# Optimization experiments

Measured on AMD Instinct MI355X. Metric: run time of the kernel, lower is better.

## Reference

```python
import jax, jax.numpy as jnp
import numpy as np


def setup_inputs() -> dict:
    key = jax.random.key(0)
    k1, k2 = jax.random.split(key)
    K, D = 512, 64
    x = jax.random.normal(k1, (64, D, 32, 32), dtype=jnp.float32)
    # torch init: uniform(-1/k, 1/k)
    weight = jax.random.uniform(k2, (D, K), dtype=jnp.float32, minval=-1.0 / K, maxval=1.0 / K)
    return {"x": x, "weight": weight}


def reference(x, weight):
    # x: [B, d, *spatial]; weight: [d, k]
    B, d = x.shape[0], x.shape[1]
    spatial = x.shape[2:]
    xf = x.reshape(B, d, -1)                      # [B, d, N]
    x2 = jnp.sum(xf * xf, axis=1)                 # [B, N]
    w2 = jnp.sum(weight * weight, axis=0)         # [k]
    dots = jnp.einsum('bdn,dk->bnk', xf, weight)  # [B, N, k]
    dist = x2[..., None] - 2.0 * dots + w2        # [B, N, k]
    argmin = jnp.argmin(dist, axis=-1)            # [B, N]
    quantized = jnp.take(weight.T, argmin, axis=0)          # [B, N, d]
    quantized = jnp.moveaxis(quantized.reshape(B, *spatial, d), -1, 1)  # [B, d, *spatial]
    return quantized, argmin.reshape(B, *spatial)
```

## Files before the change

### kernel.cpp

```cpp
#include <hip/hip_runtime.h>

#define KCODES 512
#define DDIM   64
#define NPIX   1024
#define QELEMS (64 * DDIM * NPIX)
#define PXB    64
#define FLAG_GAP 4e-5f

typedef float f32x4 __attribute__((ext_vector_type(4)));
typedef short bf16x8 __attribute__((ext_vector_type(8)));
typedef unsigned int u32;
typedef u32 u32x4 __attribute__((ext_vector_type(4)));


__device__ __forceinline__ bf16x8 pack_hi(const float* f) {
  u32x4 wds;
#pragma unroll
  for (int p = 0; p < 4; ++p) {
    u32 u0 = __float_as_uint(f[2 * p]);
    u32 u1 = __float_as_uint(f[2 * p + 1]);
    wds[p] = (u0 >> 16) | (u1 & 0xffff0000u);
  }
  return __builtin_bit_cast(bf16x8, wds);
}
__device__ __forceinline__ bf16x8 pack_lo(const float* f) {
  u32x4 wds;
#pragma unroll
  for (int p = 0; p < 4; ++p) {
    float r0 = f[2 * p]     - __uint_as_float(__float_as_uint(f[2 * p])     & 0xffff0000u);
    float r1 = f[2 * p + 1] - __uint_as_float(__float_as_uint(f[2 * p + 1]) & 0xffff0000u);
    wds[p] = (__float_as_uint(r0) >> 16) | (__float_as_uint(r1) & 0xffff0000u);
  }
  return __builtin_bit_cast(bf16x8, wds);
}

__global__ void vq_prep(const float* __restrict__ w,
                        float* __restrict__ w2f_g,
                        bf16x8* __restrict__ frag) {
#pragma clang fp contract(off)
  const int blk = blockIdx.x;
  if (blk == 32) {
    int k = threadIdx.x;
    if (k < KCODES) {
      float s = 0.0f;
      for (int d = 0; d < DDIM; ++d) {
        float v = w[d * KCODES + k];
        float p = v * v;
        s = s + p;
      }
      w2f_g[k] = s;
    }
    return;
  }
  if (threadIdx.x >= 256) return;
  const int cg   = blk;
  const int t    = threadIdx.x >> 6;
  const int lane = threadIdx.x & 63;
  const int code = cg * 16 + (lane & 15);
  const int h    = t & 1;
  float f[8];
#pragma unroll
  for (int j = 0; j < 8; ++j)
    f[j] = w[(h * 32 + (lane >> 4) * 8 + j) * KCODES + code];
  frag[(cg * 4 + t) * 64 + lane] = (t < 2) ? pack_hi(f) : pack_lo(f);
}

__global__ __launch_bounds__(256) void vq_kernel(
    const float* __restrict__ x, const float* __restrict__ w,
    const float* __restrict__ w2f_g, const bf16x8* __restrict__ frag,
    float* __restrict__ qout, float* __restrict__ aout) {
#pragma clang fp contract(off)

  __shared__ float  xs[DDIM][PXB + 1];
  __shared__ float  w2fs[KCODES];
  __shared__ int    skm[PXB];

  const int tid  = threadIdx.x;
  const int lane = tid & 63;
  const int lr   = lane & 15;
  const int lg   = lane >> 4;
  const int wid  = __builtin_amdgcn_readfirstlane(tid >> 6);
  const int b    = blockIdx.x >> 4;
  const int n0   = (blockIdx.x & 15) * PXB;
  const size_t pixbase = (size_t)blockIdx.x * PXB;
  const int px0  = wid * 16;

  {
    const float* xp = x + (size_t)b * (DDIM * NPIX) + n0;
#pragma unroll
    for (int dd = 0; dd < 16; ++dd) {
      int d = dd * 4 + wid;
      xs[d][lane] = xp[(size_t)d * NPIX + lane];
    }
  }
  w2fs[tid]       = w2f_g[tid];
  w2fs[tid + 256] = w2f_g[tid + 256];
  __syncthreads();

  bf16x8 bxh[2], bxl[2];
#pragma unroll
  for (int h = 0; h < 2; ++h) {
    float f[8];
#pragma unroll
    for (int j = 0; j < 8; ++j)
      f[j] = xs[h * 32 + lg * 8 + j][px0 + lr];
    bxh[h] = pack_hi(f);
    bxl[h] = pack_lo(f);
  }

  float m1 = 3.4e38f, m2 = 3.4e38f;
  int   i1 = 0;
#pragma unroll 2
  for (int cg = 0; cg < 32; ++cg) {
    const bf16x8* fr = frag + (size_t)cg * 4 * 64 + lane;
    bf16x8 awh0 = fr[0];
    bf16x8 awh1 = fr[64];
    bf16x8 awl0 = fr[128];
    bf16x8 awl1 = fr[192];

    f32x4 acc = {0.f, 0.f, 0.f, 0.f};
    acc = __builtin_amdgcn_mfma_f32_16x16x32_bf16(awh0, bxh[0], acc, 0, 0, 0);
    acc = __builtin_amdgcn_mfma_f32_16x16x32_bf16(awh1, bxh[1], acc, 0, 0, 0);
    acc = __builtin_amdgcn_mfma_f32_16x16x32_bf16(awl0, bxh[0], acc, 0, 0, 0);
    acc = __builtin_amdgcn_mfma_f32_16x16x32_bf16(awl1, bxh[1], acc, 0, 0, 0);
    acc = __builtin_amdgcn_mfma_f32_16x16x32_bf16(awh0, bxl[0], acc, 0, 0, 0);
    acc = __builtin_amdgcn_mfma_f32_16x16x32_bf16(awh1, bxl[1], acc, 0, 0, 0);
    acc = __builtin_amdgcn_mfma_f32_16x16x32_bf16(awl0, bxl[0], acc, 0, 0, 0);
    acc = __builtin_amdgcn_mfma_f32_16x16x32_bf16(awl1, bxl[1], acc, 0, 0, 0);
#pragma unroll
    for (int r = 0; r < 4; ++r) {
      int code = cg * 16 + lg * 4 + r;
      float s = w2fs[code] - 2.0f * acc[r];
      bool lt = s < m1;
      float om1 = m1;
      m2 = lt ? om1 : fminf(s, m2);
      m1 = lt ? s : m1;
      i1 = lt ? code : i1;
    }
  }

#pragma unroll
  for (int mi = 0; mi < 2; ++mi) {
    int mask = mi ? 32 : 16;
    float pm1 = __shfl_xor(m1, mask);
    float pm2 = __shfl_xor(m2, mask);
    int   pi1 = __shfl_xor(i1, mask);
    if (pm1 < m1) { m2 = fminf(m1, pm2); m1 = pm1; i1 = pi1; }
    else          { m2 = fminf(m2, pm1); }
  }
  if (lg == 0) skm[px0 + lr] = i1;

  unsigned long long bal = __ballot(m2 - m1 < FLAG_GAP);
  unsigned int fmask = (unsigned int)(bal & 0xFFFFu);

  while (fmask) {
    const int Lr = __builtin_ctz(fmask);
    fmask &= fmask - 1;
    const int L = px0 + Lr;
    float x2L = 0.0f;
    for (int d = 0; d < DDIM; ++d) {
      float xv = xs[d][L];
      float p = xv * xv;
      x2L = x2L + p;
    }
    const int k0 = lane * 8;
    float dots[8];
#pragma unroll
    for (int c = 0; c < 8; ++c) dots[c] = 0.f;
    for (int d = 0; d < DDIM; d += 4) {
      f32x4 wa[4][2];
      float xv[4];
#pragma unroll
      for (int u = 0; u < 4; ++u) {
        const float* wr = w + (size_t)(d + u) * KCODES + k0;
        wa[u][0] = *reinterpret_cast<const f32x4*>(wr);
        wa[u][1] = *reinterpret_cast<const f32x4*>(wr + 4);
        xv[u] = xs[d + u][L];
      }
#pragma unroll
      for (int u = 0; u < 4; ++u) {
#pragma unroll
        for (int c = 0; c < 4; ++c) {
          float p = xv[u] * wa[u][0][c];
          dots[c] = dots[c] + p;
        }
#pragma unroll
        for (int c = 0; c < 4; ++c) {
          float p = xv[u] * wa[u][1][c];
          dots[c + 4] = dots[c + 4] + p;
        }
      }
    }
    float bv = 3.4e38f;
    int   bi = 0;
#pragma unroll
    for (int c = 0; c < 8; ++c) {
      float t  = x2L - 2.0f * dots[c];
      float s2 = t + w2fs[k0 + c];
      if (s2 < bv) { bv = s2; bi = k0 + c; }
    }
#pragma unroll
    for (int off = 1; off < 64; off <<= 1) {
      float ov = __shfl_xor(bv, off);
      int   oi = __shfl_xor(bi, off);
      if (ov < bv || (ov == bv && oi < bi)) { bv = ov; bi = oi; }
    }
    if (lane == 0) skm[L] = bi;
  }

  if (lg == 0) aout[pixbase + px0 + lr] = (float)skm[px0 + lr];

  __syncthreads();

  {
    float* qp = qout + (size_t)b * (DDIM * NPIX) + n0;
#pragma unroll
    for (int i = 0; i < 16; ++i) {
      int d  = (tid >> 6) + i * 4;
      int px = tid & 63;
      qp[(size_t)d * NPIX + px] = w[d * KCODES + skm[px]];
    }
  }
}

extern "C" void kernel_launch(void* const* d_in, const int* in_sizes, int n_in,
                              void* d_out, int out_size, void* d_ws, size_t ws_size,
                              hipStream_t stream) {
  const float* x = (const float*)d_in[0];
  const float* w = (const float*)d_in[1];
  float* qout = (float*)d_out;
  float* aout = (float*)d_out + QELEMS;

  char*   wsb   = (char*)d_ws;
  float*  w2f_g = (float*)wsb;
  bf16x8* frag  = (bf16x8*)(wsb + 4096);

  vq_prep<<<33, 512, 0, stream>>>(w, w2f_g, frag);
  vq_kernel<<<(65536 / PXB), 256, 0, stream>>>(x, w, w2f_g, frag, qout, aout);
}
```

Baseline: 47.51 us.

## Halve pixels per block and split codebook search across wave pairs

Each block now handles 32 pixels instead of 64. Every pair of waves shares a 16-pixel tile and each wave scans half of the codebook groups. The two partial top-2 results are merged through shared memory, and the exact fp32 fallback for near-tie pixels is split between the pair. This doubles the grid size and raises occupancy through launch_bounds(256,8), aiming at better latency hiding, at the cost of an extra barrier, a shared-memory merge, and narrower 32-wide global loads and stores.

```diff
diff --git a/kernel.cpp b/kernel.cpp
--- a/kernel.cpp
+++ b/kernel.cpp
@@ -4,7 +4,7 @@
 #define DDIM   64
 #define NPIX   1024
 #define QELEMS (64 * DDIM * NPIX)
-#define PXB    64
+#define PXB    32
 #define FLAG_GAP 4e-5f
 
 typedef float f32x4 __attribute__((ext_vector_type(4)));
@@ -65,7 +65,7 @@
   frag[(cg * 4 + t) * 64 + lane] = (t < 2) ? pack_hi(f) : pack_lo(f);
 }
 
-__global__ __launch_bounds__(256) void vq_kernel(
+__global__ __launch_bounds__(256, 8) void vq_kernel(
     const float* __restrict__ x, const float* __restrict__ w,
     const float* __restrict__ w2f_g, const bf16x8* __restrict__ frag,
     float* __restrict__ qout, float* __restrict__ aout) {
@@ -73,6 +73,8 @@
 
   __shared__ float  xs[DDIM][PXB + 1];
   __shared__ float  w2fs[KCODES];
+  __shared__ float  hm1[2][PXB], hm2[2][PXB];
+  __shared__ int    hi1[2][PXB];
   __shared__ int    skm[PXB];
 
   const int tid  = threadIdx.x;
@@ -80,17 +82,20 @@
   const int lr   = lane & 15;
   const int lg   = lane >> 4;
   const int wid  = __builtin_amdgcn_readfirstlane(tid >> 6);
-  const int b    = blockIdx.x >> 4;
-  const int n0   = (blockIdx.x & 15) * PXB;
+  const int ch   = wid & 1;
+  const int pg   = wid >> 1;
+  const int b    = blockIdx.x >> 5;
+  const int n0   = (blockIdx.x & 31) * PXB;
   const size_t pixbase = (size_t)blockIdx.x * PXB;
-  const int px0  = wid * 16;
+  const int px0  = pg * 16;
 
   {
     const float* xp = x + (size_t)b * (DDIM * NPIX) + n0;
 #pragma unroll
-    for (int dd = 0; dd < 16; ++dd) {
-      int d = dd * 4 + wid;
-      xs[d][lane] = xp[(size_t)d * NPIX + lane];
+    for (int i = 0; i < 8; ++i) {
+      int d  = (tid >> 5) + i * 8;
+      int px = tid & 31;
+      xs[d][px] = xp[(size_t)d * NPIX + px];
     }
   }
   w2fs[tid]       = w2f_g[tid];
@@ -111,8 +116,9 @@
   float m1 = 3.4e38f, m2 = 3.4e38f;
   int   i1 = 0;
 #pragma unroll 2
-  for (int cg = 0; cg < 32; ++cg) {
-    const bf16x8* fr = frag + (size_t)cg * 4 * 64 + lane;
+  for (int i = 0; i < 16; ++i) {
+    const int cg = ch * 16 + i;
+    const bf16x8* fr = frag + (size_t)cg * 256 + lane;
     bf16x8 awh0 = fr[0];
     bf16x8 awh1 = fr[64];
     bf16x8 awl0 = fr[128];
@@ -148,76 +154,101 @@
     if (pm1 < m1) { m2 = fminf(m1, pm2); m1 = pm1; i1 = pi1; }
     else          { m2 = fminf(m2, pm1); }
   }
-  if (lg == 0) skm[px0 + lr] = i1;
-
-  unsigned long long bal = __ballot(m2 - m1 < FLAG_GAP);
+  if (lg == 0) {
+    hm1[ch][px0 + lr] = m1;
+    hm2[ch][px0 + lr] = m2;
+    hi1[ch][px0 + lr] = i1;
+  }
+  __syncthreads();
+
+  if (lane < 16) {
+    const int px = px0 + lane;
+    float a1 = hm1[0][px], a2 = hm2[0][px];
+    int   ai = hi1[0][px];
+    float b1 = hm1[1][px], b2 = hm2[1][px];
+    int   bi = hi1[1][px];
+    if (b1 < a1) { m1 = b1; m2 = fminf(a1, b2); i1 = bi; }
+    else         { m1 = a1; m2 = fminf(a2, b1); i1 = ai; }
+    if (ch == 0) skm[px] = i1;
+  }
+
+  unsigned long long bal = __ballot((lane < 16) && (m2 - m1 < FLAG_GAP));
   unsigned int fmask = (unsigned int)(bal & 0xFFFFu);
 
-  while (fmask) {
-    const int Lr = __builtin_ctz(fmask);
-    fmask &= fmask - 1;
-    const int L = px0 + Lr;
-    float x2L = 0.0f;
-    for (int d = 0; d < DDIM; ++d) {
-      float xv = xs[d][L];
-      float p = xv * xv;
-      x2L = x2L + p;
-    }
-    const int k0 = lane * 8;
-    float dots[8];
-#pragma unroll
-    for (int c = 0; c < 8; ++c) dots[c] = 0.f;
-    for (int d = 0; d < DDIM; d += 4) {
-      f32x4 wa[4][2];
-      float xv[4];
-#pragma unroll
-      for (int u = 0; u < 4; ++u) {
-        const float* wr = w + (size_t)(d + u) * KCODES + k0;
-        wa[u][0] = *reinterpret_cast<const f32x4*>(wr);
-        wa[u][1] = *reinterpret_cast<const f32x4*>(wr + 4);
-        xv[u] = xs[d + u][L];
-      }
-#pragma unroll
-      for (int u = 0; u < 4; ++u) {
-#pragma unroll
-        for (int c = 0; c < 4; ++c) {
-          float p = xv[u] * wa[u][0][c];
+  {
+    int idx = 0;
+    while (fmask) {
+      const int Lr = __builtin_ctz(fmask);
+      fmask &= fmask - 1;
+      if ((idx++ & 1) != ch) continue;
+      const int L = px0 + Lr;
+      float x2L = 0.0f;
+      for (int d = 0; d < DDIM; ++d) {
+        float xv = xs[d][L];
+        float p = xv * xv;
+        x2L = x2L + p;
+      }
+      const int k0 = lane * 8;
+      float dots[8];
+#pragma unroll
+      for (int c = 0; c < 8; ++c) dots[c] = 0.f;
+      for (int d = 0; d < DDIM; d += 2) {
+        const float* wr0 = w + (size_t)d * KCODES + k0;
+        const float* wr1 = wr0 + KCODES;
+        f32x4 wa0 = *reinterpret_cast<const f32x4*>(wr0);
+        f32x4 wb0 = *reinterpret_cast<const f32x4*>(wr0 + 4);
+        f32x4 wa1 = *reinterpret_cast<const f32x4*>(wr1);
+        f32x4 wb1 = *reinterpret_cast<const f32x4*>(wr1 + 4);
+        float xv0 = xs[d][L];
+        float xv1 = xs[d + 1][L];
+#pragma unroll
+        for (int c = 0; c < 4; ++c) {
+          float p = xv0 * wa0[c];
           dots[c] = dots[c] + p;
         }
 #pragma unroll
         for (int c = 0; c < 4; ++c) {
-          float p = xv[u] * wa[u][1][c];
+          float p = xv0 * wb0[c];
           dots[c + 4] = dots[c + 4] + p;
         }
-      }
-    }
-    float bv = 3.4e38f;
-    int   bi = 0;
-#pragma unroll
-    for (int c = 0; c < 8; ++c) {
-      float t  = x2L - 2.0f * dots[c];
-      float s2 = t + w2fs[k0 + c];
-      if (s2 < bv) { bv = s2; bi = k0 + c; }
-    }
-#pragma unroll
-    for (int off = 1; off < 64; off <<= 1) {
-      float ov = __shfl_xor(bv, off);
-      int   oi = __shfl_xor(bi, off);
-      if (ov < bv || (ov == bv && oi < bi)) { bv = ov; bi = oi; }
-    }
-    if (lane == 0) skm[L] = bi;
-  }
-
-  if (lg == 0) aout[pixbase + px0 + lr] = (float)skm[px0 + lr];
-
+#pragma unroll
+        for (int c = 0; c < 4; ++c) {
+          float p = xv1 * wa1[c];
+          dots[c] = dots[c] + p;
+        }
+#pragma unroll
+        for (int c = 0; c < 4; ++c) {
+          float p = xv1 * wb1[c];
+          dots[c + 4] = dots[c + 4] + p;
+        }
+      }
+      float bv = 3.4e38f;
+      int   bi = 0;
+#pragma unroll
+      for (int c = 0; c < 8; ++c) {
+        float t  = x2L - 2.0f * dots[c];
+        float s2 = t + w2fs[k0 + c];
+        if (s2 < bv) { bv = s2; bi = k0 + c; }
+      }
+#pragma unroll
+      for (int off = 1; off < 64; off <<= 1) {
+        float ov = __shfl_xor(bv, off);
+        int   oi = __shfl_xor(bi, off);
+        if (ov < bv || (ov == bv && oi < bi)) { bv = ov; bi = oi; }
+      }
+      if (lane == 0) skm[L] = bi;
+    }
+  }
   __syncthreads();
+
+  if (tid < PXB) aout[pixbase + tid] = (float)skm[tid];
 
   {
     float* qp = qout + (size_t)b * (DDIM * NPIX) + n0;
 #pragma unroll
-    for (int i = 0; i < 16; ++i) {
-      int d  = (tid >> 6) + i * 4;
-      int px = tid & 63;
+    for (int i = 0; i < 8; ++i) {
+      int d  = (tid >> 5) + i * 8;
+      int px = tid & 31;
       qp[(size_t)d * NPIX + px] = w[d * KCODES + skm[px]];
     }
   }
```

Measured after the change: 80.45 us. +69.3%, slower.

## Split codebook across wave pairs and reuse weight fragments over two pixel groups

Applied to the files above, without the earlier changes.

Each wave now handles 32 pixels (two 16-pixel groups) and half of the codebook. Every loaded weight fragment feeds MFMAs for both pixel groups, which halves the fragment loads per MFMA. The two codebook halves are merged through shared memory with an extra barrier, and flagged near-tie pixels are rechecked in exact fp32, split alternately between the wave pair. The min/second-min update also uses fmin/fmax and fma, which could change rounding slightly at near-ties.

```diff
diff --git a/kernel.cpp b/kernel.cpp
--- a/kernel.cpp
+++ b/kernel.cpp
@@ -73,6 +73,8 @@
 
   __shared__ float  xs[DDIM][PXB + 1];
   __shared__ float  w2fs[KCODES];
+  __shared__ float  hm1[2][PXB], hm2[2][PXB];
+  __shared__ int    hi1[2][PXB];
   __shared__ int    skm[PXB];
 
   const int tid  = threadIdx.x;
@@ -80,10 +82,12 @@
   const int lr   = lane & 15;
   const int lg   = lane >> 4;
   const int wid  = __builtin_amdgcn_readfirstlane(tid >> 6);
+  const int ch   = wid & 1;
+  const int pgh  = wid >> 1;
   const int b    = blockIdx.x >> 4;
   const int n0   = (blockIdx.x & 15) * PXB;
   const size_t pixbase = (size_t)blockIdx.x * PXB;
-  const int px0  = wid * 16;
+  const int px0  = pgh * 32;
 
   {
     const float* xp = x + (size_t)b * (DDIM * NPIX) + n0;
@@ -97,120 +101,154 @@
   w2fs[tid + 256] = w2f_g[tid + 256];
   __syncthreads();
 
-  bf16x8 bxh[2], bxl[2];
-#pragma unroll
-  for (int h = 0; h < 2; ++h) {
-    float f[8];
-#pragma unroll
-    for (int j = 0; j < 8; ++j)
-      f[j] = xs[h * 32 + lg * 8 + j][px0 + lr];
-    bxh[h] = pack_hi(f);
-    bxl[h] = pack_lo(f);
-  }
-
-  float m1 = 3.4e38f, m2 = 3.4e38f;
-  int   i1 = 0;
+  bf16x8 bxh[2][2], bxl[2][2];
+#pragma unroll
+  for (int pg = 0; pg < 2; ++pg) {
+#pragma unroll
+    for (int h = 0; h < 2; ++h) {
+      float f[8];
+#pragma unroll
+      for (int j = 0; j < 8; ++j)
+        f[j] = xs[h * 32 + lg * 8 + j][px0 + pg * 16 + lr];
+      bxh[pg][h] = pack_hi(f);
+      bxl[pg][h] = pack_lo(f);
+    }
+  }
+
+  float m1[2] = {3.4e38f, 3.4e38f};
+  float m2[2] = {3.4e38f, 3.4e38f};
+  int   i1[2] = {0, 0};
 #pragma unroll 2
-  for (int cg = 0; cg < 32; ++cg) {
-    const bf16x8* fr = frag + (size_t)cg * 4 * 64 + lane;
+  for (int i = 0; i < 16; ++i) {
+    const int cg = ch * 16 + i;
+    const bf16x8* fr = frag + (size_t)cg * 256 + lane;
     bf16x8 awh0 = fr[0];
     bf16x8 awh1 = fr[64];
     bf16x8 awl0 = fr[128];
     bf16x8 awl1 = fr[192];
 
-    f32x4 acc = {0.f, 0.f, 0.f, 0.f};
-    acc = __builtin_amdgcn_mfma_f32_16x16x32_bf16(awh0, bxh[0], acc, 0, 0, 0);
-    acc = __builtin_amdgcn_mfma_f32_16x16x32_bf16(awh1, bxh[1], acc, 0, 0, 0);
-    acc = __builtin_amdgcn_mfma_f32_16x16x32_bf16(awl0, bxh[0], acc, 0, 0, 0);
-    acc = __builtin_amdgcn_mfma_f32_16x16x32_bf16(awl1, bxh[1], acc, 0, 0, 0);
-    acc = __builtin_amdgcn_mfma_f32_16x16x32_bf16(awh0, bxl[0], acc, 0, 0, 0);
-    acc = __builtin_amdgcn_mfma_f32_16x16x32_bf16(awh1, bxl[1], acc, 0, 0, 0);
-    acc = __builtin_amdgcn_mfma_f32_16x16x32_bf16(awl0, bxl[0], acc, 0, 0, 0);
-    acc = __builtin_amdgcn_mfma_f32_16x16x32_bf16(awl1, bxl[1], acc, 0, 0, 0);
-#pragma unroll
-    for (int r = 0; r < 4; ++r) {
-      int code = cg * 16 + lg * 4 + r;
-      float s = w2fs[code] - 2.0f * acc[r];
-      bool lt = s < m1;
-      float om1 = m1;
-      m2 = lt ? om1 : fminf(s, m2);
-      m1 = lt ? s : m1;
-      i1 = lt ? code : i1;
-    }
-  }
-
-#pragma unroll
-  for (int mi = 0; mi < 2; ++mi) {
-    int mask = mi ? 32 : 16;
-    float pm1 = __shfl_xor(m1, mask);
-    float pm2 = __shfl_xor(m2, mask);
-    int   pi1 = __shfl_xor(i1, mask);
-    if (pm1 < m1) { m2 = fminf(m1, pm2); m1 = pm1; i1 = pi1; }
-    else          { m2 = fminf(m2, pm1); }
-  }
-  if (lg == 0) skm[px0 + lr] = i1;
-
-  unsigned long long bal = __ballot(m2 - m1 < FLAG_GAP);
-  unsigned int fmask = (unsigned int)(bal & 0xFFFFu);
-
-  while (fmask) {
-    const int Lr = __builtin_ctz(fmask);
-    fmask &= fmask - 1;
-    const int L = px0 + Lr;
-    float x2L = 0.0f;
-    for (int d = 0; d < DDIM; ++d) {
-      float xv = xs[d][L];
-      float p = xv * xv;
-      x2L = x2L + p;
-    }
-    const int k0 = lane * 8;
-    float dots[8];
-#pragma unroll
-    for (int c = 0; c < 8; ++c) dots[c] = 0.f;
-    for (int d = 0; d < DDIM; d += 4) {
-      f32x4 wa[4][2];
-      float xv[4];
-#pragma unroll
-      for (int u = 0; u < 4; ++u) {
-        const float* wr = w + (size_t)(d + u) * KCODES + k0;
-        wa[u][0] = *reinterpret_cast<const f32x4*>(wr);
-        wa[u][1] = *reinterpret_cast<const f32x4*>(wr + 4);
-        xv[u] = xs[d + u][L];
-      }
-#pragma unroll
-      for (int u = 0; u < 4; ++u) {
-#pragma unroll
-        for (int c = 0; c < 4; ++c) {
-          float p = xv[u] * wa[u][0][c];
-          dots[c] = dots[c] + p;
+#pragma unroll
+    for (int pg = 0; pg < 2; ++pg) {
+      f32x4 acc = {0.f, 0.f, 0.f, 0.f};
+      acc = __builtin_amdgcn_mfma_f32_16x16x32_bf16(awh0, bxh[pg][0], acc, 0, 0, 0);
+      acc = __builtin_amdgcn_mfma_f32_16x16x32_bf16(awh1, bxh[pg][1], acc, 0, 0, 0);
+      acc = __builtin_amdgcn_mfma_f32_16x16x32_bf16(awl0, bxh[pg][0], acc, 0, 0, 0);
+      acc = __builtin_amdgcn_mfma_f32_16x16x32_bf16(awl1, bxh[pg][1], acc, 0, 0, 0);
+      acc = __builtin_amdgcn_mfma_f32_16x16x32_bf16(awh0, bxl[pg][0], acc, 0, 0, 0);
+      acc = __builtin_amdgcn_mfma_f32_16x16x32_bf16(awh1, bxl[pg][1], acc, 0, 0, 0);
+      acc = __builtin_amdgcn_mfma_f32_16x16x32_bf16(awl0, bxl[pg][0], acc, 0, 0, 0);
+      acc = __builtin_amdgcn_mfma_f32_16x16x32_bf16(awl1, bxl[pg][1], acc, 0, 0, 0);
+      const int codebase = cg * 16 + lg * 4;
+#pragma unroll
+      for (int r = 0; r < 4; ++r) {
+        int code = codebase + r;
+        float s = fmaf(-2.0f, acc[r], w2fs[code]);
+        float om = m1[pg];
+        m1[pg] = fminf(om, s);
+        m2[pg] = fminf(m2[pg], fmaxf(om, s));
+        i1[pg] = (s < om) ? code : i1[pg];
+      }
+    }
+  }
+
+#pragma unroll
+  for (int pg = 0; pg < 2; ++pg) {
+#pragma unroll
+    for (int mi = 0; mi < 2; ++mi) {
+      int mask = mi ? 32 : 16;
+      float pm1 = __shfl_xor(m1[pg], mask);
+      float pm2 = __shfl_xor(m2[pg], mask);
+      int   pi1 = __shfl_xor(i1[pg], mask);
+      if (pm1 < m1[pg]) { m2[pg] = fminf(m1[pg], pm2); m1[pg] = pm1; i1[pg] = pi1; }
+      else              { m2[pg] = fminf(m2[pg], pm1); }
+    }
+    if (lg == 0) {
+      int px = px0 + pg * 16 + lr;
+      hm1[ch][px] = m1[pg];
+      hm2[ch][px] = m2[pg];
+      hi1[ch][px] = i1[pg];
+    }
+  }
+  __syncthreads();
+
+  bool flg = false;
+  if (lane < 32) {
+    const int px = px0 + lane;
+    float a1 = hm1[0][px], a2 = hm2[0][px];
+    int   ai = hi1[0][px];
+    float b1 = hm1[1][px], b2 = hm2[1][px];
+    int   bi = hi1[1][px];
+    float M1, M2;
+    int   I1;
+    if (b1 < a1) { M1 = b1; M2 = fminf(a1, b2); I1 = bi; }
+    else         { M1 = a1; M2 = fminf(a2, b1); I1 = ai; }
+    if (ch == 0) skm[px] = I1;
+    flg = (M2 - M1 < FLAG_GAP);
+  }
+  unsigned long long bal = __ballot(flg);
+  unsigned int fmask = (unsigned int)(bal & 0xFFFFFFFFu);
+
+  {
+    int idx = 0;
+    while (fmask) {
+      const int Lr = __builtin_ctz(fmask);
+      fmask &= fmask - 1;
+      if ((idx++ & 1) != ch) continue;
+      const int L = px0 + Lr;
+      float x2L = 0.0f;
+      for (int d = 0; d < DDIM; ++d) {
+        float xv = xs[d][L];
+        float p = xv * xv;
+        x2L = x2L + p;
+      }
+      const int k0 = lane * 8;
+      float dots[8];
+#pragma unroll
+      for (int c = 0; c < 8; ++c) dots[c] = 0.f;
+      for (int d = 0; d < DDIM; d += 4) {
+        f32x4 wa[4][2];
+        float xv[4];
+#pragma unroll
+        for (int u = 0; u < 4; ++u) {
+          const float* wr = w + (size_t)(d + u) * KCODES + k0;
+          wa[u][0] = *reinterpret_cast<const f32x4*>(wr);
+          wa[u][1] = *reinterpret_cast<const f32x4*>(wr + 4);
+          xv[u] = xs[d + u][L];
         }
 #pragma unroll
-        for (int c = 0; c < 4; ++c) {
-          float p = xv[u] * wa[u][1][c];
-          dots[c + 4] = dots[c + 4] + p;
+        for (int u = 0; u < 4; ++u) {
+#pragma unroll
+          for (int c = 0; c < 4; ++c) {
+            float p = xv[u] * wa[u][0][c];
+            dots[c] = dots[c] + p;
+          }
+#pragma unroll
+          for (int c = 0; c < 4; ++c) {
+            float p = xv[u] * wa[u][1][c];
+            dots[c + 4] = dots[c + 4] + p;
+          }
         }
       }
-    }
-    float bv = 3.4e38f;
-    int   bi = 0;
-#pragma unroll
-    for (int c = 0; c < 8; ++c) {
-      float t  = x2L - 2.0f * dots[c];
-      float s2 = t + w2fs[k0 + c];
-      if (s2 < bv) { bv = s2; bi = k0 + c; }
-    }
-#pragma unroll
-    for (int off = 1; off < 64; off <<= 1) {
-      float ov = __shfl_xor(bv, off);
-      int   oi = __shfl_xor(bi, off);
-      if (ov < bv || (ov == bv && oi < bi)) { bv = ov; bi = oi; }
-    }
-    if (lane == 0) skm[L] = bi;
-  }
-
-  if (lg == 0) aout[pixbase + px0 + lr] = (float)skm[px0 + lr];
-
+      float bv = 3.4e38f;
+      int   bi = 0;
+#pragma unroll
+      for (int c = 0; c < 8; ++c) {
+        float t  = x2L - 2.0f * dots[c];
+        float s2 = t + w2fs[k0 + c];
+        if (s2 < bv) { bv = s2; bi = k0 + c; }
+      }
+#pragma unroll
+      for (int off = 1; off < 64; off <<= 1) {
+        float ov = __shfl_xor(bv, off);
+        int   oi = __shfl_xor(bi, off);
+        if (ov < bv || (ov == bv && oi < bi)) { bv = ov; bi = oi; }
+      }
+      if (lane == 0) skm[L] = bi;
+    }
+  }
   __syncthreads();
+
+  if (tid < PXB) aout[pixbase + tid] = (float)skm[tid];
 
   {
     float* qp = qout + (size_t)b * (DDIM * NPIX) + n0;
```

After: 42.90 us. 9.7% less time.
